# Optimization experiments

Measured on AMD Instinct MI355X. Metric: run time of the kernel, lower is better.

The kernel has to match this reference:

```python
import jax, jax.numpy as jnp
import numpy as np

B, N, RIN, ROUT, DEMB, FIN, FE, E, ITERS = 64, 128, 32, 64, 64, 64, 16, 65536, 3
NTOT = B * N


def gnn(x, edge_index, edge_feat, Ws, Wm, We, b):
    # edge-conditioned message passing: [NTOT, Fin] -> [NTOT, Fout]
    src, dst = edge_index[0], edge_index[1]
    msg = jax.nn.relu(x[src] @ Wm + edge_feat @ We)          # [E, Fout]
    agg = jax.ops.segment_sum(msg, dst, num_segments=x.shape[0])
    return jax.nn.relu(x @ Ws + agg + b)


def setup_inputs() -> dict:
    key = jax.random.key(0)
    ks = jax.random.split(key, 20)
    s = 0.1
    return {
        "x_r": jax.random.normal(ks[0], (NTOT, FIN), jnp.float32),
        "edge_index_r": jax.random.randint(ks[1], (2, E), 0, NTOT),
        "edge_feat_r": jax.random.normal(ks[2], (E, FE), jnp.float32),
        "x_p": jax.random.normal(ks[3], (NTOT, FIN), jnp.float32),
        "edge_index_p": jax.random.randint(ks[4], (2, E), 0, NTOT),
        "edge_feat_p": jax.random.normal(ks[5], (E, FE), jnp.float32),
        "r_mask": jnp.ones((B, N), dtype=bool),
        "p_mask": jnp.ones((B, N), dtype=bool),
        # gnn_1 params (FIN -> DEMB)
        "g1_Ws": jax.random.normal(ks[6], (FIN, DEMB)) * s,
        "g1_Wm": jax.random.normal(ks[7], (FIN, DEMB)) * s,
        "g1_We": jax.random.normal(ks[8], (FE, DEMB)) * s,
        "g1_b": jnp.zeros((DEMB,), jnp.float32),
        # gnn_2 params (RIN -> ROUT)
        "g2_Ws": jax.random.normal(ks[9], (RIN, ROUT)) * s,
        "g2_Wm": jax.random.normal(ks[10], (RIN, ROUT)) * s,
        "g2_We": jax.random.normal(ks[11], (FE, ROUT)) * s,
        "g2_b": jnp.zeros((ROUT,), jnp.float32),
        # consensus mlp (ROUT -> ROUT -> 1)
        "mlp_W1": jax.random.normal(ks[12], (ROUT, ROUT)) * s,
        "mlp_b1": jnp.zeros((ROUT,), jnp.float32),
        "mlp_W2": jax.random.normal(ks[13], (ROUT, 1)) * s,
        "mlp_b2": jnp.zeros((1,), jnp.float32),
    }


def reference(x_r, edge_index_r, edge_feat_r, x_p, edge_index_p, edge_feat_p,
              r_mask, p_mask,
              g1_Ws, g1_Wm, g1_We, g1_b,
              g2_Ws, g2_Wm, g2_We, g2_b,
              mlp_W1, mlp_b1, mlp_W2, mlp_b2):
    # node embeddings via gnn_1, then dense-batch to [B, N, DEMB]
    h_r = gnn(x_r, edge_index_r, edge_feat_r, g1_Ws, g1_Wm, g1_We, g1_b).reshape(B, N, DEMB)
    h_p = gnn(x_p, edge_index_p, edge_feat_p, g1_Ws, g1_Wm, g1_We, g1_b).reshape(B, N, DEMB)

    M_hat = jnp.einsum('brd,bpd->brp', h_r, h_p)             # [B, N_r, N_p]
    M_mask = r_mask[:, :, None] & p_mask[:, None, :]
    M_0 = jax.nn.softmax(M_hat, axis=-1).reshape(NTOT, N)    # packed (full mask)

    rkey = jax.random.key(42)
    for it in range(ITERS):
        M = jax.nn.softmax(M_hat, axis=-1)
        rf_r = jax.random.normal(jax.random.fold_in(rkey, it), (B, N, RIN), jnp.float32)
        rf_p = jnp.einsum('brp,bri->bpi', M, rf_r)           # M^T @ rand
        o_r = gnn(rf_r.reshape(NTOT, RIN), edge_index_r, edge_feat_r,
                  g2_Ws, g2_Wm, g2_We, g2_b).reshape(B, N, ROUT)
        o_p = gnn(rf_p.reshape(NTOT, RIN), edge_index_p, edge_feat_p,
                  g2_Ws, g2_Wm, g2_We, g2_b).reshape(B, N, ROUT)
        D = o_r[:, :, None, :] - o_p[:, None, :, :]          # [B, N_r, N_p, ROUT]
        upd = (jax.nn.relu(D @ mlp_W1 + mlp_b1) @ mlp_W2 + mlp_b2)[..., 0]
        M_hat = M_hat + jnp.where(M_mask, upd, 0.0)

    M_T = jax.nn.softmax(M_hat, axis=-1).reshape(NTOT, N)
    return (M_0, M_T)
```

## Files before the change

kernel.cpp:

```cpp
#include <hip/hip_runtime.h>

constexpr int kE = 65536, kNTOT = 8192;

__host__ __device__ __forceinline__ void tf_round(unsigned& x0, unsigned& x1, int r) {
  x0 += x1;
  x1 = (x1 << r) | (x1 >> (32 - r));
  x1 ^= x0;
}
__host__ __device__ __forceinline__ void tf2x32(unsigned k0, unsigned k1,
                                                unsigned& x0, unsigned& x1) {
  unsigned ks2 = k0 ^ k1 ^ 0x1BD11BDAu;
  x0 += k0; x1 += k1;
  tf_round(x0,x1,13); tf_round(x0,x1,15); tf_round(x0,x1,26); tf_round(x0,x1,6);
  x0 += k1; x1 += ks2 + 1u;
  tf_round(x0,x1,17); tf_round(x0,x1,29); tf_round(x0,x1,16); tf_round(x0,x1,24);
  x0 += ks2; x1 += k0 + 2u;
  tf_round(x0,x1,13); tf_round(x0,x1,15); tf_round(x0,x1,26); tf_round(x0,x1,6);
  x0 += k0; x1 += k1 + 3u;
  tf_round(x0,x1,17); tf_round(x0,x1,29); tf_round(x0,x1,16); tf_round(x0,x1,24);
  x0 += k1; x1 += ks2 + 4u;
  tf_round(x0,x1,13); tf_round(x0,x1,15); tf_round(x0,x1,26); tf_round(x0,x1,6);
  x0 += ks2; x1 += k0 + 5u;
}

__device__ __forceinline__ float bits_to_normal(unsigned bits) {
  float f = __uint_as_float((bits >> 9) | 0x3f800000u) - 1.0f;
  const float LO = -0.99999994f;
  float u = fmaf(f, 2.0f, LO);
  u = fmaxf(u, LO);
  float w = -log1pf(-u * u);
  float p;
  if (w < 5.0f) {
    w -= 2.5f;
    p = 2.81022636e-08f;
    p = fmaf(p, w, 3.43273939e-07f);
    p = fmaf(p, w, -3.5233877e-06f);
    p = fmaf(p, w, -4.39150654e-06f);
    p = fmaf(p, w, 0.00021858087f);
    p = fmaf(p, w, -0.00125372503f);
    p = fmaf(p, w, -0.00417768164f);
    p = fmaf(p, w, 0.246640727f);
    p = fmaf(p, w, 1.50140941f);
  } else {
    w = sqrtf(w) - 3.0f;
    p = -0.000200214257f;
    p = fmaf(p, w, 0.000100950558f);
    p = fmaf(p, w, 0.00134934322f);
    p = fmaf(p, w, -0.00367342844f);
    p = fmaf(p, w, 0.00573950773f);
    p = fmaf(p, w, -0.0076224613f);
    p = fmaf(p, w, 0.00943887047f);
    p = fmaf(p, w, 1.00167406f);
    p = fmaf(p, w, 2.83297682f);
  }
  return 1.41421356f * (p * u);
}

__device__ __forceinline__ float redmax32(float v) {
#pragma unroll
  for (int o = 16; o > 0; o >>= 1) v = fmaxf(v, __shfl_xor(v, o));
  return v;
}
__device__ __forceinline__ float redsum32(float v) {
#pragma unroll
  for (int o = 16; o > 0; o >>= 1) v += __shfl_xor(v, o);
  return v;
}

__global__ __launch_bounds__(256) void hist_kern(const int* __restrict__ eiR,
                                                 const int* __restrict__ eiP,
                                                 int* __restrict__ offR,
                                                 int* __restrict__ offP,
                                                 float* __restrict__ aggz) {
  int i = blockIdx.x * 256 + threadIdx.x;
  float4 z4 = make_float4(0.f, 0.f, 0.f, 0.f);
  float4* z = reinterpret_cast<float4*>(aggz) + i * 2;
  z[0] = z4; z[1] = z4;
  const int* ei = (i < kE) ? eiR : eiP;
  int* off = (i < kE) ? offR : offP;
  int e = i & (kE - 1);
  atomicAdd(&off[ei[kE + e]], 1);
}

__global__ __launch_bounds__(256) void scan_kern(int* __restrict__ offR,
                                                 int* __restrict__ offP) {
  int* off = blockIdx.x ? offP : offR;
  int t = threadIdx.x;
  int base = t * 32;
  int v[32];
#pragma unroll
  for (int i = 0; i < 32; ++i) v[i] = off[base + i];
  int sum = 0;
#pragma unroll
  for (int i = 0; i < 32; ++i) sum += v[i];
  int lane = t & 63, w = t >> 6;
  int incl = sum;
#pragma unroll
  for (int o = 1; o < 64; o <<= 1) {
    int y = __shfl_up(incl, o);
    if (lane >= o) incl += y;
  }
  __shared__ int wsum[4];
  if (lane == 63) wsum[w] = incl;
  __syncthreads();
  int woff = 0;
#pragma unroll
  for (int i = 0; i < 4; ++i) if (i < w) woff += wsum[i];
  int running = woff + incl - sum;
#pragma unroll
  for (int i = 0; i < 32; ++i) {
    off[base + i] = running;
    running += v[i];
  }
}

__global__ __launch_bounds__(256) void scatter_kern(
    const int* __restrict__ eiR, const int* __restrict__ eiP,
    int* __restrict__ offR, int* __restrict__ offP,
    int* __restrict__ permR, int* __restrict__ permP,
    int* __restrict__ srcsR, int* __restrict__ srcsP,
    int* __restrict__ dstsR, int* __restrict__ dstsP) {
  int i = blockIdx.x * 256 + threadIdx.x;
  const int* ei = (i < kE) ? eiR : eiP;
  int* off = (i < kE) ? offR : offP;
  int* perm = (i < kE) ? permR : permP;
  int* srcs = (i < kE) ? srcsR : srcsP;
  int* dsts = (i < kE) ? dstsR : dstsP;
  int e = i & (kE - 1);
  int dst = ei[kE + e];
  int pos = atomicAdd(&off[dst], 1);
  perm[pos] = e;
  srcs[pos] = ei[e];
  dsts[pos] = dst;
}

template <int KX>
__global__ __launch_bounds__(256) void msg_gemm(
    const float* __restrict__ xR, const float* __restrict__ efR,
    const int* __restrict__ srcsR, const int* __restrict__ permR,
    const int* __restrict__ dstsR, float* __restrict__ aggR,
    const float* __restrict__ xP, const float* __restrict__ efP,
    const int* __restrict__ srcsP, const int* __restrict__ permP,
    const int* __restrict__ dstsP, float* __restrict__ aggP,
    const float* __restrict__ Wm, const float* __restrict__ We) {
  constexpr int KT = KX + 16;
  constexpr int SA_ROWS = (KT > 64) ? KT : 64;
  __shared__ float sA[SA_ROWS][68];
  __shared__ float sW[KT][68];
  __shared__ int sDst[64];
  __shared__ int sSrc[64];
  __shared__ int sPerm[64];
  bool isP = blockIdx.x >= 1024;
  const float* x = isP ? xP : xR;
  const float* ef = isP ? efP : efR;
  const int* srcs = isP ? srcsP : srcsR;
  const int* perm = isP ? permP : permR;
  const int* dsts = isP ? dstsP : dstsR;
  float* agg = isP ? aggP : aggR;
  int i0 = (blockIdx.x & 1023) * 64;
  int t = threadIdx.x;
#pragma unroll
  for (int idx = 0; idx < KT * 64 / 1024; ++idx) {
    int q = t * 4 + idx * 1024;
    int k = q >> 6, j = q & 63;
    const float* sp = (k < KX) ? (Wm + k * 64 + j) : (We + (k - KX) * 64 + j);
    float4 v = *reinterpret_cast<const float4*>(sp);
    *reinterpret_cast<float4*>(&sW[k][j]) = v;
  }
  if (t < 64) {
    sDst[t] = dsts[i0 + t];
    sSrc[t] = srcs[i0 + t];
    sPerm[t] = perm[i0 + t];
  }
  __syncthreads();
  {
    int l = t & 3;
    int g = t >> 2;
    int rb = g >> 2;
    int kq = g & 3;
    int gbase = (t & 63) & ~3;
#pragma unroll
    for (int idx = 0; idx < KT / 16; ++idx) {
      int k4 = idx * 16 + kq * 4;
      int r = rb * 4 + l;
      const float* rptr = (k4 < KX) ? (x + (size_t)sSrc[r] * KX + k4)
                                    : (ef + (size_t)sPerm[r] * 16 + (k4 - KX));
      float4 v = *reinterpret_cast<const float4*>(rptr);
      float vc[4] = {v.x, v.y, v.z, v.w};
      float out[4];
#pragma unroll
      for (int c = 0; c < 4; ++c) {
        float val = vc[(l - c) & 3];
        out[(l + c) & 3] = __shfl(val, gbase + ((l + c) & 3), 64);
      }
      *reinterpret_cast<float4*>(&sA[k4 + l][rb * 4]) =
          make_float4(out[0], out[1], out[2], out[3]);
    }
  }
  __syncthreads();
  int tn = (t & 15) * 4;
  int tj = (t >> 4) * 4;
  float acc[4][4] = {};
#pragma unroll 8
  for (int k = 0; k < KT; ++k) {
    float4 a = *reinterpret_cast<const float4*>(&sA[k][tn]);
    float4 b = *reinterpret_cast<const float4*>(&sW[k][tj]);
    acc[0][0] = fmaf(a.x, b.x, acc[0][0]); acc[0][1] = fmaf(a.x, b.y, acc[0][1]);
    acc[0][2] = fmaf(a.x, b.z, acc[0][2]); acc[0][3] = fmaf(a.x, b.w, acc[0][3]);
    acc[1][0] = fmaf(a.y, b.x, acc[1][0]); acc[1][1] = fmaf(a.y, b.y, acc[1][1]);
    acc[1][2] = fmaf(a.y, b.z, acc[1][2]); acc[1][3] = fmaf(a.y, b.w, acc[1][3]);
    acc[2][0] = fmaf(a.z, b.x, acc[2][0]); acc[2][1] = fmaf(a.z, b.y, acc[2][1]);
    acc[2][2] = fmaf(a.z, b.z, acc[2][2]); acc[2][3] = fmaf(a.z, b.w, acc[2][3]);
    acc[3][0] = fmaf(a.w, b.x, acc[3][0]); acc[3][1] = fmaf(a.w, b.y, acc[3][1]);
    acc[3][2] = fmaf(a.w, b.z, acc[3][2]); acc[3][3] = fmaf(a.w, b.w, acc[3][3]);
  }
  __syncthreads();
#pragma unroll
  for (int i = 0; i < 4; ++i) {
    *reinterpret_cast<float4*>(&sA[tn + i][tj]) =
        make_float4(fmaxf(acc[i][0], 0.f), fmaxf(acc[i][1], 0.f),
                    fmaxf(acc[i][2], 0.f), fmaxf(acc[i][3], 0.f));
  }
  __syncthreads();
  int col = t & 63;
  int r0l = (t >> 6) * 16;
  float run = 0.f;
  int rd = sDst[r0l];
#pragma unroll
  for (int r = 0; r < 16; ++r) {
    int d = sDst[r0l + r];
    if (d != rd) {
      unsafeAtomicAdd(&agg[(size_t)rd * 64 + col], run);
      run = 0.f; rd = d;
    }
    run += sA[r0l + r][col];
  }
  unsafeAtomicAdd(&agg[(size_t)rd * 64 + col], run);
}

__global__ __launch_bounds__(256) void node1_gemm(
    const float* __restrict__ xR, float* __restrict__ aggR, float* __restrict__ hR,
    const float* __restrict__ xP, float* __restrict__ aggP, float* __restrict__ hP,
    const float* __restrict__ Ws, const float* __restrict__ bias) {
  __shared__ float sX[64][68];
  __shared__ float sW[64][68];
  bool isP = blockIdx.x >= 128;
  const float* x = isP ? xP : xR;
  float* agg = isP ? aggP : aggR;
  float* h = isP ? hP : hR;
  int n0 = (blockIdx.x & 127) * 64;
  int t = threadIdx.x;
#pragma unroll
  for (int idx = 0; idx < 4; ++idx) {
    int q = t * 4 + idx * 1024;
    int k = q >> 6, j = q & 63;
    *reinterpret_cast<float4*>(&sW[k][j]) = *reinterpret_cast<const float4*>(Ws + q);
    float4 v = *reinterpret_cast<const float4*>(x + (size_t)n0 * 64 + q);
    sX[j + 0][k] = v.x; sX[j + 1][k] = v.y; sX[j + 2][k] = v.z; sX[j + 3][k] = v.w;
  }
  __syncthreads();
  int tn = (t & 15) * 4, tj = (t >> 4) * 4;
  float acc[4][4] = {};
#pragma unroll 8
  for (int k = 0; k < 64; ++k) {
    float4 a = *reinterpret_cast<const float4*>(&sX[k][tn]);
    float4 b = *reinterpret_cast<const float4*>(&sW[k][tj]);
    acc[0][0] = fmaf(a.x, b.x, acc[0][0]); acc[0][1] = fmaf(a.x, b.y, acc[0][1]);
    acc[0][2] = fmaf(a.x, b.z, acc[0][2]); acc[0][3] = fmaf(a.x, b.w, acc[0][3]);
    acc[1][0] = fmaf(a.y, b.x, acc[1][0]); acc[1][1] = fmaf(a.y, b.y, acc[1][1]);
    acc[1][2] = fmaf(a.y, b.z, acc[1][2]); acc[1][3] = fmaf(a.y, b.w, acc[1][3]);
    acc[2][0] = fmaf(a.z, b.x, acc[2][0]); acc[2][1] = fmaf(a.z, b.y, acc[2][1]);
    acc[2][2] = fmaf(a.z, b.z, acc[2][2]); acc[2][3] = fmaf(a.z, b.w, acc[2][3]);
    acc[3][0] = fmaf(a.w, b.x, acc[3][0]); acc[3][1] = fmaf(a.w, b.y, acc[3][1]);
    acc[3][2] = fmaf(a.w, b.z, acc[3][2]); acc[3][3] = fmaf(a.w, b.w, acc[3][3]);
  }
  float4 bv = *reinterpret_cast<const float4*>(bias + tj);
  float4 z4 = make_float4(0.f, 0.f, 0.f, 0.f);
#pragma unroll
  for (int i = 0; i < 4; ++i) {
    int n = n0 + tn + i;
    float4 g = *reinterpret_cast<const float4*>(&agg[(size_t)n * 64 + tj]);
    *reinterpret_cast<float4*>(&agg[(size_t)n * 64 + tj]) = z4;
    float4 o;
    o.x = fmaxf(acc[i][0] + g.x + bv.x, 0.f);
    o.y = fmaxf(acc[i][1] + g.y + bv.y, 0.f);
    o.z = fmaxf(acc[i][2] + g.z + bv.z, 0.f);
    o.w = fmaxf(acc[i][3] + g.w + bv.w, 0.f);
    *reinterpret_cast<float4*>(&h[(size_t)n * 64 + tj]) = o;
  }
}

__global__ __launch_bounds__(256) void mhat_soft(
    const float* __restrict__ hR, const float* __restrict__ hP,
    float* __restrict__ Mhat, float* __restrict__ Msoft, float* __restrict__ M0out,
    float* __restrict__ rfr, unsigned fk0, unsigned fk1) {
  __shared__ float hr[16][66];
  __shared__ float hp[128][66];
  int gid = blockIdx.x, t = threadIdx.x;
  int gtid = (gid << 8) + t;
#pragma unroll
  for (int q = 0; q < 2; ++q) {
    unsigned i = (unsigned)gtid + (unsigned)q * 131072u;
    unsigned a0 = 0u, a1 = i;
    tf2x32(fk0, fk1, a0, a1);
    rfr[i] = bits_to_normal(a0 ^ a1);
  }
  int b = gid >> 3, r0 = (gid & 7) * 16;
  const float* hrG = hR + ((size_t)(b * 128 + r0)) * 64;
  {
    int q = t * 4; int r = q >> 6, d = q & 63;
    float4 v = *reinterpret_cast<const float4*>(hrG + q);
    hr[r][d] = v.x; hr[r][d + 1] = v.y; hr[r][d + 2] = v.z; hr[r][d + 3] = v.w;
  }
  const float* hpG = hP + (size_t)b * 128 * 64;
#pragma unroll
  for (int rep = 0; rep < 8; ++rep) {
    int q = (rep * 256 + t) * 4; int p = q >> 6, d = q & 63;
    float4 v = *reinterpret_cast<const float4*>(hpG + q);
    hp[p][d] = v.x; hp[p][d + 1] = v.y; hp[p][d + 2] = v.z; hp[p][d + 3] = v.w;
  }
  __syncthreads();
  int tx = t & 31, ty = t >> 5;
  float acc[2][4] = {};
  for (int d = 0; d < 64; ++d) {
    float a0 = hr[ty][d], a1 = hr[ty + 8][d];
    float q0 = hp[tx][d], q1 = hp[tx + 32][d], q2 = hp[tx + 64][d], q3 = hp[tx + 96][d];
    acc[0][0] = fmaf(a0, q0, acc[0][0]); acc[0][1] = fmaf(a0, q1, acc[0][1]);
    acc[0][2] = fmaf(a0, q2, acc[0][2]); acc[0][3] = fmaf(a0, q3, acc[0][3]);
    acc[1][0] = fmaf(a1, q0, acc[1][0]); acc[1][1] = fmaf(a1, q1, acc[1][1]);
    acc[1][2] = fmaf(a1, q2, acc[1][2]); acc[1][3] = fmaf(a1, q3, acc[1][3]);
  }
#pragma unroll
  for (int ii = 0; ii < 2; ++ii) {
    int r = r0 + ty + 8 * ii;
    float* mrow = Mhat + ((size_t)(b * 128 + r)) * 128;
    mrow[tx] = acc[ii][0]; mrow[tx + 32] = acc[ii][1];
    mrow[tx + 64] = acc[ii][2]; mrow[tx + 96] = acc[ii][3];
    float mx = redmax32(fmaxf(fmaxf(acc[ii][0], acc[ii][1]), fmaxf(acc[ii][2], acc[ii][3])));
    float e0 = __expf(acc[ii][0] - mx), e1 = __expf(acc[ii][1] - mx);
    float e2 = __expf(acc[ii][2] - mx), e3 = __expf(acc[ii][3] - mx);
    float inv = 1.0f / redsum32(e0 + e1 + e2 + e3);
    float* srow = Msoft + ((size_t)(b * 128 + r)) * 128;
    srow[tx] = e0 * inv; srow[tx + 32] = e1 * inv;
    srow[tx + 64] = e2 * inv; srow[tx + 96] = e3 * inv;
    float* orow = M0out + ((size_t)(b * 128 + r)) * 128;
    orow[tx] = e0 * inv; orow[tx + 32] = e1 * inv;
    orow[tx + 64] = e2 * inv; orow[tx + 96] = e3 * inv;
  }
}

__global__ __launch_bounds__(256) void rfp_kern(
    const float* __restrict__ Msoft, const float* __restrict__ rfr,
    float* __restrict__ rfp) {
  __shared__ float rr[128][36];
  int b = blockIdx.x >> 3, p0 = (blockIdx.x & 7) * 16;
  int t = threadIdx.x;
  const float* rfG = rfr + (size_t)b * 4096;
#pragma unroll
  for (int rep = 0; rep < 4; ++rep) {
    int q = (rep * 256 + t) * 4; int r = q >> 5, i = q & 31;
    float4 v = *reinterpret_cast<const float4*>(rfG + q);
    rr[r][i] = v.x; rr[r][i + 1] = v.y; rr[r][i + 2] = v.z; rr[r][i + 3] = v.w;
  }
  __syncthreads();
  int pl = t & 15, ih = (t >> 4) * 2;
  int p = p0 + pl;
  const float* Mcol = Msoft + (size_t)b * 16384 + p;
  float a0 = 0.f, a1 = 0.f;
#pragma unroll 8
  for (int r = 0; r < 128; ++r) {
    float m = Mcol[(size_t)r * 128];
    a0 = fmaf(m, rr[r][ih], a0);
    a1 = fmaf(m, rr[r][ih + 1], a1);
  }
  float* dst = rfp + ((size_t)(b * 128 + p)) * 32 + ih;
  dst[0] = a0; dst[1] = a1;
}

__global__ __launch_bounds__(256) void node2u_gemm(
    const float* __restrict__ rfR, float* __restrict__ aggR, float* __restrict__ uR,
    const float* __restrict__ rfP, float* __restrict__ aggP, float* __restrict__ uP,
    const float* __restrict__ Ws2, const float* __restrict__ g2b,
    const float* __restrict__ W1, const float* __restrict__ b1) {
  __shared__ float sRF[32][68];
  __shared__ float sW2[32][68];
  __shared__ float sW1[64][68];
  __shared__ float sO[64][68];
  bool isP = blockIdx.x >= 128;
  const float* rf = isP ? rfP : rfR;
  float* agg = isP ? aggP : aggR;
  float* u = isP ? uP : uR;
  int n0 = (blockIdx.x & 127) * 64;
  int t = threadIdx.x;
#pragma unroll
  for (int idx = 0; idx < 4; ++idx) {
    int q = t * 4 + idx * 1024;
    *reinterpret_cast<float4*>(&sW1[q >> 6][q & 63]) = *reinterpret_cast<const float4*>(W1 + q);
  }
#pragma unroll
  for (int idx = 0; idx < 2; ++idx) {
    int q = t * 4 + idx * 1024;
    *reinterpret_cast<float4*>(&sW2[q >> 6][q & 63]) = *reinterpret_cast<const float4*>(Ws2 + q);
    int r = q >> 5, kk = q & 31;
    float4 v = *reinterpret_cast<const float4*>(rf + (size_t)(n0 + r) * 32 + kk);
    sRF[kk][r] = v.x; sRF[kk + 1][r] = v.y; sRF[kk + 2][r] = v.z; sRF[kk + 3][r] = v.w;
  }
  __syncthreads();
  int tn = (t & 15) * 4, tj = (t >> 4) * 4;
  float acc[4][4] = {};
#pragma unroll 8
  for (int k = 0; k < 32; ++k) {
    float4 a = *reinterpret_cast<const float4*>(&sRF[k][tn]);
    float4 b = *reinterpret_cast<const float4*>(&sW2[k][tj]);
    acc[0][0] = fmaf(a.x, b.x, acc[0][0]); acc[0][1] = fmaf(a.x, b.y, acc[0][1]);
    acc[0][2] = fmaf(a.x, b.z, acc[0][2]); acc[0][3] = fmaf(a.x, b.w, acc[0][3]);
    acc[1][0] = fmaf(a.y, b.x, acc[1][0]); acc[1][1] = fmaf(a.y, b.y, acc[1][1]);
    acc[1][2] = fmaf(a.y, b.z, acc[1][2]); acc[1][3] = fmaf(a.y, b.w, acc[1][3]);
    acc[2][0] = fmaf(a.z, b.x, acc[2][0]); acc[2][1] = fmaf(a.z, b.y, acc[2][1]);
    acc[2][2] = fmaf(a.z, b.z, acc[2][2]); acc[2][3] = fmaf(a.z, b.w, acc[2][3]);
    acc[3][0] = fmaf(a.w, b.x, acc[3][0]); acc[3][1] = fmaf(a.w, b.y, acc[3][1]);
    acc[3][2] = fmaf(a.w, b.z, acc[3][2]); acc[3][3] = fmaf(a.w, b.w, acc[3][3]);
  }
  float4 bg = *reinterpret_cast<const float4*>(g2b + tj);
  float4 z4 = make_float4(0.f, 0.f, 0.f, 0.f);
#pragma unroll
  for (int i = 0; i < 4; ++i) {
    int n = n0 + tn + i;
    float4 g = *reinterpret_cast<const float4*>(&agg[(size_t)n * 64 + tj]);
    *reinterpret_cast<float4*>(&agg[(size_t)n * 64 + tj]) = z4;
    sO[tj + 0][tn + i] = fmaxf(acc[i][0] + g.x + bg.x, 0.f);
    sO[tj + 1][tn + i] = fmaxf(acc[i][1] + g.y + bg.y, 0.f);
    sO[tj + 2][tn + i] = fmaxf(acc[i][2] + g.z + bg.z, 0.f);
    sO[tj + 3][tn + i] = fmaxf(acc[i][3] + g.w + bg.w, 0.f);
  }
  __syncthreads();
  float acc2[4][4] = {};
#pragma unroll 8
  for (int k = 0; k < 64; ++k) {
    float4 a = *reinterpret_cast<const float4*>(&sO[k][tn]);
    float4 b = *reinterpret_cast<const float4*>(&sW1[k][tj]);
    acc2[0][0] = fmaf(a.x, b.x, acc2[0][0]); acc2[0][1] = fmaf(a.x, b.y, acc2[0][1]);
    acc2[0][2] = fmaf(a.x, b.z, acc2[0][2]); acc2[0][3] = fmaf(a.x, b.w, acc2[0][3]);
    acc2[1][0] = fmaf(a.y, b.x, acc2[1][0]); acc2[1][1] = fmaf(a.y, b.y, acc2[1][1]);
    acc2[1][2] = fmaf(a.y, b.z, acc2[1][2]); acc2[1][3] = fmaf(a.y, b.w, acc2[1][3]);
    acc2[2][0] = fmaf(a.z, b.x, acc2[2][0]); acc2[2][1] = fmaf(a.z, b.y, acc2[2][1]);
    acc2[2][2] = fmaf(a.z, b.z, acc2[2][2]); acc2[2][3] = fmaf(a.z, b.w, acc2[2][3]);
    acc2[3][0] = fmaf(a.w, b.x, acc2[3][0]); acc2[3][1] = fmaf(a.w, b.y, acc2[3][1]);
    acc2[3][2] = fmaf(a.w, b.z, acc2[3][2]); acc2[3][3] = fmaf(a.w, b.w, acc2[3][3]);
  }
  float4 b1v = make_float4(0.f, 0.f, 0.f, 0.f);
  if (!isP) b1v = *reinterpret_cast<const float4*>(b1 + tj);
#pragma unroll
  for (int i = 0; i < 4; ++i) {
    int n = n0 + tn + i;
    float4 o;
    o.x = acc2[i][0] + b1v.x; o.y = acc2[i][1] + b1v.y;
    o.z = acc2[i][2] + b1v.z; o.w = acc2[i][3] + b1v.w;
    *reinterpret_cast<float4*>(&u[(size_t)n * 64 + tj]) = o;
  }
}

__global__ __launch_bounds__(256) void upd_soft(
    const float* __restrict__ uR, const float* __restrict__ uP,
    const float* __restrict__ W2, const float* __restrict__ b2p,
    float* __restrict__ Mhat, float* __restrict__ softDst,
    int writeMhat, float* __restrict__ rfr, int doRng,
    unsigned fk0, unsigned fk1) {
  __shared__ float sur[16][66];
  __shared__ float sup[128][66];
  __shared__ float sw2[64];
  int gid = blockIdx.x, t = threadIdx.x;
  int b = gid >> 3, r0 = (gid & 7) * 16;
  const float* urG = uR + ((size_t)(b * 128 + r0)) * 64;
  {
    int q = t * 4; int r = q >> 6, d = q & 63;
    float4 v = *reinterpret_cast<const float4*>(urG + q);
    sur[r][d] = v.x; sur[r][d + 1] = v.y; sur[r][d + 2] = v.z; sur[r][d + 3] = v.w;
  }
  const float* upG = uP + (size_t)b * 128 * 64;
#pragma unroll
  for (int rep = 0; rep < 8; ++rep) {
    int q = (rep * 256 + t) * 4; int p = q >> 6, d = q & 63;
    float4 v = *reinterpret_cast<const float4*>(upG + q);
    sup[p][d] = v.x; sup[p][d + 1] = v.y; sup[p][d + 2] = v.z; sup[p][d + 3] = v.w;
  }
  if (t < 64) sw2[t] = W2[t];
  __syncthreads();
  int tx = t & 31, ty = t >> 5;
  float acc[2][4] = {};
  for (int j = 0; j < 64; ++j) {
    float w2v = sw2[j];
    float a0 = sur[ty][j], a1 = sur[ty + 8][j];
    float q0 = sup[tx][j], q1 = sup[tx + 32][j], q2 = sup[tx + 64][j], q3 = sup[tx + 96][j];
    acc[0][0] = fmaf(fmaxf(a0 - q0, 0.f), w2v, acc[0][0]);
    acc[0][1] = fmaf(fmaxf(a0 - q1, 0.f), w2v, acc[0][1]);
    acc[0][2] = fmaf(fmaxf(a0 - q2, 0.f), w2v, acc[0][2]);
    acc[0][3] = fmaf(fmaxf(a0 - q3, 0.f), w2v, acc[0][3]);
    acc[1][0] = fmaf(fmaxf(a1 - q0, 0.f), w2v, acc[1][0]);
    acc[1][1] = fmaf(fmaxf(a1 - q1, 0.f), w2v, acc[1][1]);
    acc[1][2] = fmaf(fmaxf(a1 - q2, 0.f), w2v, acc[1][2]);
    acc[1][3] = fmaf(fmaxf(a1 - q3, 0.f), w2v, acc[1][3]);
  }
  float b2v = b2p[0];
#pragma unroll
  for (int ii = 0; ii < 2; ++ii) {
    int r = r0 + ty + 8 * ii;
    float* mrow = Mhat + ((size_t)(b * 128 + r)) * 128;
    float m0 = mrow[tx] + acc[ii][0] + b2v;
    float m1 = mrow[tx + 32] + acc[ii][1] + b2v;
    float m2 = mrow[tx + 64] + acc[ii][2] + b2v;
    float m3 = mrow[tx + 96] + acc[ii][3] + b2v;
    if (writeMhat) {
      mrow[tx] = m0; mrow[tx + 32] = m1; mrow[tx + 64] = m2; mrow[tx + 96] = m3;
    }
    float mx = redmax32(fmaxf(fmaxf(m0, m1), fmaxf(m2, m3)));
    float e0 = __expf(m0 - mx), e1 = __expf(m1 - mx);
    float e2 = __expf(m2 - mx), e3 = __expf(m3 - mx);
    float inv = 1.0f / redsum32(e0 + e1 + e2 + e3);
    float* srow = softDst + ((size_t)(b * 128 + r)) * 128;
    srow[tx] = e0 * inv; srow[tx + 32] = e1 * inv;
    srow[tx + 64] = e2 * inv; srow[tx + 96] = e3 * inv;
  }
  if (doRng) {
    int gtid = (gid << 8) + t;
#pragma unroll
    for (int q = 0; q < 2; ++q) {
      unsigned i = (unsigned)gtid + (unsigned)q * 131072u;
      unsigned a0 = 0u, a1 = i;
      tf2x32(fk0, fk1, a0, a1);
      rfr[i] = bits_to_normal(a0 ^ a1);
    }
  }
}

extern "C" void kernel_launch(void* const* d_in, const int* in_sizes, int n_in,
                              void* d_out, int out_size, void* d_ws, size_t ws_size,
                              hipStream_t stream) {
  (void)in_sizes; (void)n_in; (void)out_size; (void)ws_size;
  const float* x_r  = (const float*)d_in[0];
  const int*   ei_r = (const int*)d_in[1];
  const float* ef_r = (const float*)d_in[2];
  const float* x_p  = (const float*)d_in[3];
  const int*   ei_p = (const int*)d_in[4];
  const float* ef_p = (const float*)d_in[5];
  const float* g1_Ws = (const float*)d_in[8];
  const float* g1_Wm = (const float*)d_in[9];
  const float* g1_We = (const float*)d_in[10];
  const float* g1_b  = (const float*)d_in[11];
  const float* g2_Ws = (const float*)d_in[12];
  const float* g2_Wm = (const float*)d_in[13];
  const float* g2_We = (const float*)d_in[14];
  const float* g2_b  = (const float*)d_in[15];
  const float* W1 = (const float*)d_in[16];
  const float* b1 = (const float*)d_in[17];
  const float* W2 = (const float*)d_in[18];
  const float* b2 = (const float*)d_in[19];
  float* out = (float*)d_out;

  float* ws = (float*)d_ws;
  float* h_r   = ws;
  float* h_p   = h_r + 524288;
  float* Mhat  = h_p + 524288;
  float* Msoft = Mhat + 1048576;
  float* rfr   = Msoft + 1048576;
  float* rfp   = rfr + 262144;
  float* u_r   = rfp + 262144;
  float* u_p   = u_r + 524288;
  float* agg_r = u_p + 524288;
  float* agg_p = agg_r + 524288;
  int* ib      = (int*)(agg_p + 524288);
  int* off_r  = ib;
  int* off_p  = off_r + 8192;
  int* perm_r = off_p + 8192;
  int* perm_p = perm_r + 65536;
  int* srcs_r = perm_p + 65536;
  int* srcs_p = srcs_r + 65536;
  int* dsts_r = srcs_p + 65536;
  int* dsts_p = dsts_r + 65536;

  unsigned fk0[3], fk1[3];
  for (int it = 0; it < 3; ++it) {
    unsigned a = 0u, c = (unsigned)it;
    tf2x32(0u, 42u, a, c);
    fk0[it] = a; fk1[it] = c;
  }

  hipMemsetAsync(off_r, 0, 2 * 8192 * sizeof(int), stream);
  hist_kern<<<512, 256, 0, stream>>>(ei_r, ei_p, off_r, off_p, agg_r);
  scan_kern<<<2, 256, 0, stream>>>(off_r, off_p);
  scatter_kern<<<512, 256, 0, stream>>>(ei_r, ei_p, off_r, off_p,
                                        perm_r, perm_p, srcs_r, srcs_p,
                                        dsts_r, dsts_p);

  msg_gemm<64><<<2048, 256, 0, stream>>>(x_r, ef_r, srcs_r, perm_r, dsts_r, agg_r,
                                         x_p, ef_p, srcs_p, perm_p, dsts_p, agg_p,
                                         g1_Wm, g1_We);
  node1_gemm<<<256, 256, 0, stream>>>(x_r, agg_r, h_r, x_p, agg_p, h_p, g1_Ws, g1_b);
  mhat_soft<<<512, 256, 0, stream>>>(h_r, h_p, Mhat, Msoft, out, rfr, fk0[0], fk1[0]);

  for (int it = 0; it < 3; ++it) {
    rfp_kern<<<512, 256, 0, stream>>>(Msoft, rfr, rfp);
    msg_gemm<32><<<2048, 256, 0, stream>>>(rfr, ef_r, srcs_r, perm_r, dsts_r, agg_r,
                                           rfp, ef_p, srcs_p, perm_p, dsts_p, agg_p,
                                           g2_Wm, g2_We);
    node2u_gemm<<<256, 256, 0, stream>>>(rfr, agg_r, u_r, rfp, agg_p, u_p,
                                         g2_Ws, g2_b, W1, b1);
    int last = (it == 2);
    upd_soft<<<512, 256, 0, stream>>>(u_r, u_p, W2, b2, Mhat,
                                      last ? (out + 1048576) : Msoft,
                                      !last,
                                      rfr, !last,
                                      fk0[it < 2 ? it + 1 : 0], fk1[it < 2 ? it + 1 : 0]);
  }
}
```

Baseline: 297.3 us.

## Precompute node-level x@Wm before gather and fuse M^T·rand into softmax kernels

The message GEMM is split in two. The x@Wm product is now computed once per node in a new xw_gemm and gathered per edge, so msg_edge only multiplies the 16-wide edge features by We, instead of multiplying the gathered x rows per edge. The rfp computation (M^T @ rand) is fused into mhat_soft and upd_soft using per-tile partial sums and atomics, which removes the Msoft buffer round-trip and the separate rfp kernel. rfp must now be zeroed in hist_kern and node2u_gemm. The float atomics make the rfp summation order nondeterministic.

```diff
diff --git a/kernel.cpp b/kernel.cpp
--- a/kernel.cpp
+++ b/kernel.cpp
@@ -71,11 +71,13 @@
                                                  const int* __restrict__ eiP,
                                                  int* __restrict__ offR,
                                                  int* __restrict__ offP,
-                                                 float* __restrict__ aggz) {
+                                                 float* __restrict__ aggz,
+                                                 float* __restrict__ rfpz) {
   int i = blockIdx.x * 256 + threadIdx.x;
   float4 z4 = make_float4(0.f, 0.f, 0.f, 0.f);
   float4* z = reinterpret_cast<float4*>(aggz) + i * 2;
   z[0] = z4; z[1] = z4;
+  reinterpret_cast<float2*>(rfpz)[i] = make_float2(0.f, 0.f);
   const int* ei = (i < kE) ? eiR : eiP;
   int* off = (i < kE) ? offR : offP;
   int e = i & (kE - 1);
@@ -134,76 +136,33 @@
   dsts[pos] = dst;
 }
 
-template <int KX>
-__global__ __launch_bounds__(256) void msg_gemm(
-    const float* __restrict__ xR, const float* __restrict__ efR,
-    const int* __restrict__ srcsR, const int* __restrict__ permR,
-    const int* __restrict__ dstsR, float* __restrict__ aggR,
-    const float* __restrict__ xP, const float* __restrict__ efP,
-    const int* __restrict__ srcsP, const int* __restrict__ permP,
-    const int* __restrict__ dstsP, float* __restrict__ aggP,
-    const float* __restrict__ Wm, const float* __restrict__ We) {
-  constexpr int KT = KX + 16;
-  constexpr int SA_ROWS = (KT > 64) ? KT : 64;
-  __shared__ float sA[SA_ROWS][68];
-  __shared__ float sW[KT][68];
-  __shared__ int sDst[64];
-  __shared__ int sSrc[64];
-  __shared__ int sPerm[64];
-  bool isP = blockIdx.x >= 1024;
-  const float* x = isP ? xP : xR;
-  const float* ef = isP ? efP : efR;
-  const int* srcs = isP ? srcsP : srcsR;
-  const int* perm = isP ? permP : permR;
-  const int* dsts = isP ? dstsP : dstsR;
-  float* agg = isP ? aggP : aggR;
-  int i0 = (blockIdx.x & 1023) * 64;
+template <int KK>
+__global__ __launch_bounds__(256) void xw_gemm(
+    const float* __restrict__ inR, const float* __restrict__ inP,
+    float* __restrict__ xwR, float* __restrict__ xwP,
+    const float* __restrict__ W) {
+  __shared__ float sX[KK][68];
+  __shared__ float sW[KK][68];
+  bool isP = blockIdx.x >= 128;
+  const float* in = isP ? inP : inR;
+  float* xw = isP ? xwP : xwR;
+  int n0 = (blockIdx.x & 127) * 64;
   int t = threadIdx.x;
 #pragma unroll
-  for (int idx = 0; idx < KT * 64 / 1024; ++idx) {
+  for (int idx = 0; idx < KK * 64 / 1024; ++idx) {
     int q = t * 4 + idx * 1024;
     int k = q >> 6, j = q & 63;
-    const float* sp = (k < KX) ? (Wm + k * 64 + j) : (We + (k - KX) * 64 + j);
-    float4 v = *reinterpret_cast<const float4*>(sp);
-    *reinterpret_cast<float4*>(&sW[k][j]) = v;
-  }
-  if (t < 64) {
-    sDst[t] = dsts[i0 + t];
-    sSrc[t] = srcs[i0 + t];
-    sPerm[t] = perm[i0 + t];
-  }
-  __syncthreads();
-  {
-    int l = t & 3;
-    int g = t >> 2;
-    int rb = g >> 2;
-    int kq = g & 3;
-    int gbase = (t & 63) & ~3;
-#pragma unroll
-    for (int idx = 0; idx < KT / 16; ++idx) {
-      int k4 = idx * 16 + kq * 4;
-      int r = rb * 4 + l;
-      const float* rptr = (k4 < KX) ? (x + (size_t)sSrc[r] * KX + k4)
-                                    : (ef + (size_t)sPerm[r] * 16 + (k4 - KX));
-      float4 v = *reinterpret_cast<const float4*>(rptr);
-      float vc[4] = {v.x, v.y, v.z, v.w};
-      float out[4];
-#pragma unroll
-      for (int c = 0; c < 4; ++c) {
-        float val = vc[(l - c) & 3];
-        out[(l + c) & 3] = __shfl(val, gbase + ((l + c) & 3), 64);
-      }
-      *reinterpret_cast<float4*>(&sA[k4 + l][rb * 4]) =
-          make_float4(out[0], out[1], out[2], out[3]);
-    }
-  }
-  __syncthreads();
-  int tn = (t & 15) * 4;
-  int tj = (t >> 4) * 4;
+    *reinterpret_cast<float4*>(&sW[k][j]) = *reinterpret_cast<const float4*>(W + q);
+    int r = q / KK, kk = q & (KK - 1);
+    float4 v = *reinterpret_cast<const float4*>(in + (size_t)n0 * KK + q);
+    sX[kk][r] = v.x; sX[kk + 1][r] = v.y; sX[kk + 2][r] = v.z; sX[kk + 3][r] = v.w;
+  }
+  __syncthreads();
+  int tn = (t & 15) * 4, tj = (t >> 4) * 4;
   float acc[4][4] = {};
 #pragma unroll 8
-  for (int k = 0; k < KT; ++k) {
-    float4 a = *reinterpret_cast<const float4*>(&sA[k][tn]);
+  for (int k = 0; k < KK; ++k) {
+    float4 a = *reinterpret_cast<const float4*>(&sX[k][tn]);
     float4 b = *reinterpret_cast<const float4*>(&sW[k][tj]);
     acc[0][0] = fmaf(a.x, b.x, acc[0][0]); acc[0][1] = fmaf(a.x, b.y, acc[0][1]);
     acc[0][2] = fmaf(a.x, b.z, acc[0][2]); acc[0][3] = fmaf(a.x, b.w, acc[0][3]);
@@ -214,12 +173,89 @@
     acc[3][0] = fmaf(a.w, b.x, acc[3][0]); acc[3][1] = fmaf(a.w, b.y, acc[3][1]);
     acc[3][2] = fmaf(a.w, b.z, acc[3][2]); acc[3][3] = fmaf(a.w, b.w, acc[3][3]);
   }
-  __syncthreads();
 #pragma unroll
   for (int i = 0; i < 4; ++i) {
-    *reinterpret_cast<float4*>(&sA[tn + i][tj]) =
-        make_float4(fmaxf(acc[i][0], 0.f), fmaxf(acc[i][1], 0.f),
-                    fmaxf(acc[i][2], 0.f), fmaxf(acc[i][3], 0.f));
+    *reinterpret_cast<float4*>(&xw[(size_t)(n0 + tn + i) * 64 + tj]) =
+        make_float4(acc[i][0], acc[i][1], acc[i][2], acc[i][3]);
+  }
+}
+
+__global__ __launch_bounds__(256) void msg_edge(
+    const float* __restrict__ xwR, const float* __restrict__ efR,
+    const int* __restrict__ srcsR, const int* __restrict__ permR,
+    const int* __restrict__ dstsR, float* __restrict__ aggR,
+    const float* __restrict__ xwP, const float* __restrict__ efP,
+    const int* __restrict__ srcsP, const int* __restrict__ permP,
+    const int* __restrict__ dstsP, float* __restrict__ aggP,
+    const float* __restrict__ We) {
+  __shared__ float sEF[16][68];
+  __shared__ float sW[16][68];
+  __shared__ float sOut[64][68];
+  __shared__ int sDst[64];
+  __shared__ int sSrc[64];
+  __shared__ int sPerm[64];
+  bool isP = blockIdx.x >= 1024;
+  const float* xw = isP ? xwP : xwR;
+  const float* ef = isP ? efP : efR;
+  const int* srcs = isP ? srcsP : srcsR;
+  const int* perm = isP ? permP : permR;
+  const int* dsts = isP ? dstsP : dstsR;
+  float* agg = isP ? aggP : aggR;
+  int i0 = (blockIdx.x & 1023) * 64;
+  int t = threadIdx.x;
+  {
+    int q = t * 4;
+    int k = q >> 6, j = q & 63;
+    *reinterpret_cast<float4*>(&sW[k][j]) = *reinterpret_cast<const float4*>(We + q);
+  }
+  if (t < 64) {
+    sDst[t] = dsts[i0 + t];
+    sSrc[t] = srcs[i0 + t];
+    sPerm[t] = perm[i0 + t];
+  }
+  __syncthreads();
+  {
+    int l = t & 3;
+    int g = t >> 2;
+    int rb = g >> 2;
+    int kq = g & 3;
+    int gbase = (t & 63) & ~3;
+    int k4 = kq * 4;
+    int r = rb * 4 + l;
+    const float* rptr = ef + (size_t)sPerm[r] * 16 + k4;
+    float4 v = *reinterpret_cast<const float4*>(rptr);
+    float vc[4] = {v.x, v.y, v.z, v.w};
+    float out[4];
+#pragma unroll
+    for (int c = 0; c < 4; ++c) {
+      float val = vc[(l - c) & 3];
+      out[(l + c) & 3] = __shfl(val, gbase + ((l + c) & 3), 64);
+    }
+    *reinterpret_cast<float4*>(&sEF[k4 + l][rb * 4]) =
+        make_float4(out[0], out[1], out[2], out[3]);
+  }
+  __syncthreads();
+  int tn = (t & 15) * 4, tj = (t >> 4) * 4;
+  float acc[4][4] = {};
+#pragma unroll
+  for (int k = 0; k < 16; ++k) {
+    float4 a = *reinterpret_cast<const float4*>(&sEF[k][tn]);
+    float4 b = *reinterpret_cast<const float4*>(&sW[k][tj]);
+    acc[0][0] = fmaf(a.x, b.x, acc[0][0]); acc[0][1] = fmaf(a.x, b.y, acc[0][1]);
+    acc[0][2] = fmaf(a.x, b.z, acc[0][2]); acc[0][3] = fmaf(a.x, b.w, acc[0][3]);
+    acc[1][0] = fmaf(a.y, b.x, acc[1][0]); acc[1][1] = fmaf(a.y, b.y, acc[1][1]);
+    acc[1][2] = fmaf(a.y, b.z, acc[1][2]); acc[1][3] = fmaf(a.y, b.w, acc[1][3]);
+    acc[2][0] = fmaf(a.z, b.x, acc[2][0]); acc[2][1] = fmaf(a.z, b.y, acc[2][1]);
+    acc[2][2] = fmaf(a.z, b.z, acc[2][2]); acc[2][3] = fmaf(a.z, b.w, acc[2][3]);
+    acc[3][0] = fmaf(a.w, b.x, acc[3][0]); acc[3][1] = fmaf(a.w, b.y, acc[3][1]);
+    acc[3][2] = fmaf(a.w, b.z, acc[3][2]); acc[3][3] = fmaf(a.w, b.w, acc[3][3]);
+  }
+#pragma unroll
+  for (int i = 0; i < 4; ++i) {
+    float4 g = *reinterpret_cast<const float4*>(xw + (size_t)sSrc[tn + i] * 64 + tj);
+    *reinterpret_cast<float4*>(&sOut[tn + i][tj]) =
+        make_float4(fmaxf(acc[i][0] + g.x, 0.f), fmaxf(acc[i][1] + g.y, 0.f),
+                    fmaxf(acc[i][2] + g.z, 0.f), fmaxf(acc[i][3] + g.w, 0.f));
   }
   __syncthreads();
   int col = t & 63;
@@ -233,7 +269,7 @@
       unsafeAtomicAdd(&agg[(size_t)rd * 64 + col], run);
       run = 0.f; rd = d;
     }
-    run += sA[r0l + r][col];
+    run += sOut[r0l + r][col];
   }
   unsafeAtomicAdd(&agg[(size_t)rd * 64 + col], run);
 }
@@ -290,22 +326,51 @@
   }
 }
 
+__device__ __forceinline__ void rfp_partial(const float sm[16][128],
+                                            const float rfb[16][32],
+                                            float* __restrict__ rfpB, int t) {
+  float rfc[16];
+  int iw = t & 31;
+#pragma unroll
+  for (int r = 0; r < 16; ++r) rfc[r] = rfb[r][iw];
+#pragma unroll
+  for (int rep = 0; rep < 16; ++rep) {
+    int p = rep * 8 + (t >> 5);
+    float a = 0.f;
+#pragma unroll
+    for (int r = 0; r < 16; ++r) a = fmaf(sm[r][p], rfc[r], a);
+    unsafeAtomicAdd(&rfpB[p * 32 + iw], a);
+  }
+}
+
+__device__ __forceinline__ void gen_rfr_tile(float* __restrict__ rfr,
+                                             float rfb[16][32], int b, int r0,
+                                             int t, unsigned fk0, unsigned fk1) {
+  unsigned base = (unsigned)((b * 128 + r0) * 32);
+#pragma unroll
+  for (int q = 0; q < 2; ++q) {
+    unsigned j = (unsigned)(q * 256 + t);
+    unsigned i = base + j;
+    unsigned a0 = 0u, a1 = i;
+    tf2x32(fk0, fk1, a0, a1);
+    float v = bits_to_normal(a0 ^ a1);
+    rfr[i] = v;
+    rfb[j >> 5][j & 31] = v;
+  }
+}
+
 __global__ __launch_bounds__(256) void mhat_soft(
     const float* __restrict__ hR, const float* __restrict__ hP,
-    float* __restrict__ Mhat, float* __restrict__ Msoft, float* __restrict__ M0out,
-    float* __restrict__ rfr, unsigned fk0, unsigned fk1) {
+    float* __restrict__ Mhat, float* __restrict__ M0out,
+    float* __restrict__ rfr, float* __restrict__ rfp,
+    unsigned fk0, unsigned fk1) {
   __shared__ float hr[16][66];
   __shared__ float hp[128][66];
+  __shared__ float sm[16][128];
+  __shared__ float rfb[16][32];
   int gid = blockIdx.x, t = threadIdx.x;
-  int gtid = (gid << 8) + t;
-#pragma unroll
-  for (int q = 0; q < 2; ++q) {
-    unsigned i = (unsigned)gtid + (unsigned)q * 131072u;
-    unsigned a0 = 0u, a1 = i;
-    tf2x32(fk0, fk1, a0, a1);
-    rfr[i] = bits_to_normal(a0 ^ a1);
-  }
   int b = gid >> 3, r0 = (gid & 7) * 16;
+  gen_rfr_tile(rfr, rfb, b, r0, t, fk0, fk1);
   const float* hrG = hR + ((size_t)(b * 128 + r0)) * 64;
   {
     int q = t * 4; int r = q >> 6, d = q & 63;
@@ -340,48 +405,23 @@
     float e0 = __expf(acc[ii][0] - mx), e1 = __expf(acc[ii][1] - mx);
     float e2 = __expf(acc[ii][2] - mx), e3 = __expf(acc[ii][3] - mx);
     float inv = 1.0f / redsum32(e0 + e1 + e2 + e3);
-    float* srow = Msoft + ((size_t)(b * 128 + r)) * 128;
-    srow[tx] = e0 * inv; srow[tx + 32] = e1 * inv;
-    srow[tx + 64] = e2 * inv; srow[tx + 96] = e3 * inv;
     float* orow = M0out + ((size_t)(b * 128 + r)) * 128;
     orow[tx] = e0 * inv; orow[tx + 32] = e1 * inv;
     orow[tx + 64] = e2 * inv; orow[tx + 96] = e3 * inv;
-  }
-}
-
-__global__ __launch_bounds__(256) void rfp_kern(
-    const float* __restrict__ Msoft, const float* __restrict__ rfr,
-    float* __restrict__ rfp) {
-  __shared__ float rr[128][36];
-  int b = blockIdx.x >> 3, p0 = (blockIdx.x & 7) * 16;
-  int t = threadIdx.x;
-  const float* rfG = rfr + (size_t)b * 4096;
-#pragma unroll
-  for (int rep = 0; rep < 4; ++rep) {
-    int q = (rep * 256 + t) * 4; int r = q >> 5, i = q & 31;
-    float4 v = *reinterpret_cast<const float4*>(rfG + q);
-    rr[r][i] = v.x; rr[r][i + 1] = v.y; rr[r][i + 2] = v.z; rr[r][i + 3] = v.w;
-  }
-  __syncthreads();
-  int pl = t & 15, ih = (t >> 4) * 2;
-  int p = p0 + pl;
-  const float* Mcol = Msoft + (size_t)b * 16384 + p;
-  float a0 = 0.f, a1 = 0.f;
-#pragma unroll 8
-  for (int r = 0; r < 128; ++r) {
-    float m = Mcol[(size_t)r * 128];
-    a0 = fmaf(m, rr[r][ih], a0);
-    a1 = fmaf(m, rr[r][ih + 1], a1);
-  }
-  float* dst = rfp + ((size_t)(b * 128 + p)) * 32 + ih;
-  dst[0] = a0; dst[1] = a1;
+    int rl = ty + 8 * ii;
+    sm[rl][tx] = e0 * inv; sm[rl][tx + 32] = e1 * inv;
+    sm[rl][tx + 64] = e2 * inv; sm[rl][tx + 96] = e3 * inv;
+  }
+  __syncthreads();
+  rfp_partial(sm, rfb, rfp + (size_t)b * 4096, t);
 }
 
 __global__ __launch_bounds__(256) void node2u_gemm(
     const float* __restrict__ rfR, float* __restrict__ aggR, float* __restrict__ uR,
     const float* __restrict__ rfP, float* __restrict__ aggP, float* __restrict__ uP,
     const float* __restrict__ Ws2, const float* __restrict__ g2b,
-    const float* __restrict__ W1, const float* __restrict__ b1) {
+    const float* __restrict__ W1, const float* __restrict__ b1,
+    float* __restrict__ rfp_clear) {
   __shared__ float sRF[32][68];
   __shared__ float sW2[32][68];
   __shared__ float sW1[64][68];
@@ -406,6 +446,11 @@
     sRF[kk][r] = v.x; sRF[kk + 1][r] = v.y; sRF[kk + 2][r] = v.z; sRF[kk + 3][r] = v.w;
   }
   __syncthreads();
+  if (isP) {
+    float4 z4 = make_float4(0.f, 0.f, 0.f, 0.f);
+    float4* rz = reinterpret_cast<float4*>(rfp_clear + (size_t)n0 * 32);
+    rz[t * 2] = z4; rz[t * 2 + 1] = z4;
+  }
   int tn = (t & 15) * 4, tj = (t >> 4) * 4;
   float acc[4][4] = {};
 #pragma unroll 8
@@ -463,14 +508,17 @@
 __global__ __launch_bounds__(256) void upd_soft(
     const float* __restrict__ uR, const float* __restrict__ uP,
     const float* __restrict__ W2, const float* __restrict__ b2p,
-    float* __restrict__ Mhat, float* __restrict__ softDst,
-    int writeMhat, float* __restrict__ rfr, int doRng,
+    float* __restrict__ Mhat, float* __restrict__ outLast, int last,
+    float* __restrict__ rfr, float* __restrict__ rfp,
     unsigned fk0, unsigned fk1) {
   __shared__ float sur[16][66];
   __shared__ float sup[128][66];
   __shared__ float sw2[64];
+  __shared__ float sm[16][128];
+  __shared__ float rfb[16][32];
   int gid = blockIdx.x, t = threadIdx.x;
   int b = gid >> 3, r0 = (gid & 7) * 16;
+  if (!last) gen_rfr_tile(rfr, rfb, b, r0, t, fk0, fk1);
   const float* urG = uR + ((size_t)(b * 128 + r0)) * 64;
   {
     int q = t * 4; int r = q >> 6, d = q & 63;
@@ -510,26 +558,26 @@
     float m1 = mrow[tx + 32] + acc[ii][1] + b2v;
     float m2 = mrow[tx + 64] + acc[ii][2] + b2v;
     float m3 = mrow[tx + 96] + acc[ii][3] + b2v;
-    if (writeMhat) {
+    if (!last) {
       mrow[tx] = m0; mrow[tx + 32] = m1; mrow[tx + 64] = m2; mrow[tx + 96] = m3;
     }
     float mx = redmax32(fmaxf(fmaxf(m0, m1), fmaxf(m2, m3)));
     float e0 = __expf(m0 - mx), e1 = __expf(m1 - mx);
     float e2 = __expf(m2 - mx), e3 = __expf(m3 - mx);
     float inv = 1.0f / redsum32(e0 + e1 + e2 + e3);
-    float* srow = softDst + ((size_t)(b * 128 + r)) * 128;
-    srow[tx] = e0 * inv; srow[tx + 32] = e1 * inv;
-    srow[tx + 64] = e2 * inv; srow[tx + 96] = e3 * inv;
-  }
-  if (doRng) {
-    int gtid = (gid << 8) + t;
-#pragma unroll
-    for (int q = 0; q < 2; ++q) {
-      unsigned i = (unsigned)gtid + (unsigned)q * 131072u;
-      unsigned a0 = 0u, a1 = i;
-      tf2x32(fk0, fk1, a0, a1);
-      rfr[i] = bits_to_normal(a0 ^ a1);
+    if (last) {
+      float* orow = outLast + ((size_t)(b * 128 + r)) * 128;
+      orow[tx] = e0 * inv; orow[tx + 32] = e1 * inv;
+      orow[tx + 64] = e2 * inv; orow[tx + 96] = e3 * inv;
+    } else {
+      int rl = ty + 8 * ii;
+      sm[rl][tx] = e0 * inv; sm[rl][tx + 32] = e1 * inv;
+      sm[rl][tx + 64] = e2 * inv; sm[rl][tx + 96] = e3 * inv;
     }
+  }
+  if (!last) {
+    __syncthreads();
+    rfp_partial(sm, rfb, rfp + (size_t)b * 4096, t);
   }
 }
 
@@ -561,14 +609,15 @@
   float* h_r   = ws;
   float* h_p   = h_r + 524288;
   float* Mhat  = h_p + 524288;
-  float* Msoft = Mhat + 1048576;
-  float* rfr   = Msoft + 1048576;
+  float* rfr   = Mhat + 1048576;
   float* rfp   = rfr + 262144;
   float* u_r   = rfp + 262144;
   float* u_p   = u_r + 524288;
   float* agg_r = u_p + 524288;
   float* agg_p = agg_r + 524288;
-  int* ib      = (int*)(agg_p + 524288);
+  float* xw_r  = agg_p + 524288;
+  float* xw_p  = xw_r + 524288;
+  int* ib      = (int*)(xw_p + 524288);
   int* off_r  = ib;
   int* off_p  = off_r + 8192;
   int* perm_r = off_p + 8192;
@@ -586,30 +635,30 @@
   }
 
   hipMemsetAsync(off_r, 0, 2 * 8192 * sizeof(int), stream);
-  hist_kern<<<512, 256, 0, stream>>>(ei_r, ei_p, off_r, off_p, agg_r);
+  hist_kern<<<512, 256, 0, stream>>>(ei_r, ei_p, off_r, off_p, agg_r, rfp);
   scan_kern<<<2, 256, 0, stream>>>(off_r, off_p);
   scatter_kern<<<512, 256, 0, stream>>>(ei_r, ei_p, off_r, off_p,
                                         perm_r, perm_p, srcs_r, srcs_p,
                                         dsts_r, dsts_p);
 
-  msg_gemm<64><<<2048, 256, 0, stream>>>(x_r, ef_r, srcs_r, perm_r, dsts_r, agg_r,
-                                         x_p, ef_p, srcs_p, perm_p, dsts_p, agg_p,
-                                         g1_Wm, g1_We);
+  xw_gemm<64><<<256, 256, 0, stream>>>(x_r, x_p, xw_r, xw_p, g1_Wm);
+  msg_edge<<<2048, 256, 0, stream>>>(xw_r, ef_r, srcs_r, perm_r, dsts_r, agg_r,
+                                     xw_p, ef_p, srcs_p, perm_p, dsts_p, agg_p,
+                                     g1_We);
   node1_gemm<<<256, 256, 0, stream>>>(x_r, agg_r, h_r, x_p, agg_p, h_p, g1_Ws, g1_b);
-  mhat_soft<<<512, 256, 0, stream>>>(h_r, h_p, Mhat, Msoft, out, rfr, fk0[0], fk1[0]);
+  mhat_soft<<<512, 256, 0, stream>>>(h_r, h_p, Mhat, out, rfr, rfp, fk0[0], fk1[0]);
 
   for (int it = 0; it < 3; ++it) {
-    rfp_kern<<<512, 256, 0, stream>>>(Msoft, rfr, rfp);
-    msg_gemm<32><<<2048, 256, 0, stream>>>(rfr, ef_r, srcs_r, perm_r, dsts_r, agg_r,
-                                           rfp, ef_p, srcs_p, perm_p, dsts_p, agg_p,
-                                           g2_Wm, g2_We);
+    xw_gemm<32><<<256, 256, 0, stream>>>(rfr, rfp, xw_r, xw_p, g2_Wm);
+    msg_edge<<<2048, 256, 0, stream>>>(xw_r, ef_r, srcs_r, perm_r, dsts_r, agg_r,
+                                       xw_p, ef_p, srcs_p, perm_p, dsts_p, agg_p,
+                                       g2_We);
     node2u_gemm<<<256, 256, 0, stream>>>(rfr, agg_r, u_r, rfp, agg_p, u_p,
-                                         g2_Ws, g2_b, W1, b1);
+                                         g2_Ws, g2_b, W1, b1, rfp);
     int last = (it == 2);
     upd_soft<<<512, 256, 0, stream>>>(u_r, u_p, W2, b2, Mhat,
-                                      last ? (out + 1048576) : Msoft,
-                                      !last,
-                                      rfr, !last,
+                                      out + 1048576, last,
+                                      rfr, rfp,
                                       fk0[it < 2 ? it + 1 : 0], fk1[it < 2 ? it + 1 : 0]);
   }
 }
```

Result: faster. 284.2 us (-4.4%).
